# Kernel optimization log

Measured on AMD Instinct MI355X. Metric: run time of the kernel, lower is better.

The kernel has to match this reference:

```python
import jax, jax.numpy as jnp
import numpy as np

D_MODEL = 2048
H = 8
DK = D_MODEL // H          # 256
EXPAND = 2
D_INNER = EXPAND * D_MODEL  # 4096
D_STATE = 16
D_CONV = 4
DT_RANK = D_MODEL // 16     # 128
B_SZ = 8
L = 1024


def setup_inputs() -> dict:
    key = jax.random.key(0)
    ks = jax.random.split(key, 20)
    s = 0.02
    inp = {
        "imageFeature": jax.random.normal(ks[0], (B_SZ, L, D_MODEL), jnp.float32),
        "kf": jax.random.normal(ks[1], (B_SZ, L, D_MODEL), jnp.float32),
        # MHA params (4 linears with bias)
        "Wq": jax.random.normal(ks[2], (D_MODEL, D_MODEL), jnp.float32) * s,
        "bq": jnp.zeros((D_MODEL,), jnp.float32),
        "Wk": jax.random.normal(ks[3], (D_MODEL, D_MODEL), jnp.float32) * s,
        "bk": jnp.zeros((D_MODEL,), jnp.float32),
        "Wv": jax.random.normal(ks[4], (D_MODEL, D_MODEL), jnp.float32) * s,
        "bv": jnp.zeros((D_MODEL,), jnp.float32),
        "Wo": jax.random.normal(ks[5], (D_MODEL, D_MODEL), jnp.float32) * s,
        "bo": jnp.zeros((D_MODEL,), jnp.float32),
        # Mamba params
        "W_in": jax.random.normal(ks[6], (D_MODEL, 2 * D_INNER), jnp.float32) * s,
        "conv_w": jax.random.normal(ks[7], (D_INNER, D_CONV), jnp.float32) * s,
        "conv_b": jnp.zeros((D_INNER,), jnp.float32),
        "W_extra": jax.random.normal(ks[8], (D_MODEL, D_INNER), jnp.float32) * s,
        "W_xproj": jax.random.normal(ks[9], (D_INNER, DT_RANK + 2 * D_STATE), jnp.float32) * s,
        "W_dt": jax.random.normal(ks[10], (DT_RANK, D_INNER), jnp.float32) * s,
        "b_dt": jnp.full((D_INNER,), -4.6, jnp.float32),  # softplus(-4.6) ~ 0.01 init dt
        "A_log": jnp.log(jnp.broadcast_to(jnp.arange(1, D_STATE + 1, dtype=jnp.float32), (D_INNER, D_STATE))),
        "D_skip": jnp.ones((D_INNER,), jnp.float32),
        "W_out": jax.random.normal(ks[11], (D_INNER, D_MODEL), jnp.float32) * s,
    }
    return inp


def _mha(x, Wq, bq, Wk, bk, Wv, bv, Wo, bo):
    B, T, _ = x.shape
    q = (x @ Wq + bq).reshape(B, T, H, DK)
    k = (x @ Wk + bk).reshape(B, T, H, DK)
    v = (x @ Wv + bv).reshape(B, T, H, DK)
    scores = jnp.einsum("bqhd,bkhd->bhqk", q, k) / jnp.sqrt(jnp.float32(DK))
    attn = jax.nn.softmax(scores, axis=-1)
    out = jnp.einsum("bhqk,bkhd->bqhd", attn, v).reshape(B, T, D_MODEL)
    return out @ Wo + bo


def _mamba_cross(x_in, kf, W_in, conv_w, conv_b, W_extra, W_xproj, W_dt, b_dt, A_log, D_skip, W_out):
    B, T, _ = x_in.shape
    xz = x_in @ W_in                       # (B,T,2*D_INNER)
    x, z = jnp.split(xz, 2, axis=-1)
    # causal depthwise conv1d (kernel D_CONV)
    x_pad = jnp.pad(x, ((0, 0), (D_CONV - 1, 0), (0, 0)))
    x_conv = sum(conv_w[:, k] * x_pad[:, k:k + T, :] for k in range(D_CONV)) + conv_b
    x = jax.nn.silu(x_conv)               # (B,T,D_INNER)
    # dt/B/C conditioned on extra_emb (cross path)
    e = kf @ W_extra                       # (B,T,D_INNER)
    dbc = e @ W_xproj                      # (B,T,DT_RANK+2*D_STATE)
    dt = jax.nn.softplus(dbc[..., :DT_RANK] @ W_dt + b_dt)        # (B,T,D_INNER)
    Bt = dbc[..., DT_RANK:DT_RANK + D_STATE]                      # (B,T,N)
    Ct = dbc[..., DT_RANK + D_STATE:]                             # (B,T,N)
    A = -jnp.exp(A_log)                    # (D_INNER, D_STATE)

    def step(h, inputs):
        x_t, dt_t, B_t, C_t = inputs       # (B,D),(B,D),(B,N),(B,N)
        dA = jnp.exp(dt_t[..., None] * A)              # (B,D,N)
        h = dA * h + dt_t[..., None] * B_t[:, None, :] * x_t[..., None]
        y_t = jnp.einsum("bdn,bn->bd", h, C_t)
        return h, y_t

    h0 = jnp.zeros((B, D_INNER, D_STATE), x.dtype)
    xs = (x.transpose(1, 0, 2), dt.transpose(1, 0, 2),
          Bt.transpose(1, 0, 2), Ct.transpose(1, 0, 2))
    _, ys = jax.lax.scan(step, h0, xs)     # ys: (T,B,D_INNER)
    y = ys.transpose(1, 0, 2) + D_skip * x
    y = y * jax.nn.silu(z)
    return y @ W_out


def reference(imageFeature, kf, Wq, bq, Wk, bk, Wv, bv, Wo, bo,
              W_in, conv_w, conv_b, W_extra, W_xproj, W_dt, b_dt,
              A_log, D_skip, W_out):
    att_feats = _mha(imageFeature, Wq, bq, Wk, bk, Wv, bv, Wo, bo)
    src = _mamba_cross(imageFeature, kf, W_in, conv_w, conv_b, W_extra,
                       W_xproj, W_dt, b_dt, A_log, D_skip, W_out)
    return jnp.stack([att_feats, src])     # (2,B,T,D_MODEL)
```

## Files before the change

### kernel.cpp

```cpp
#include <hip/hip_runtime.h>
#include <math.h>

#define NH 8
#define DKH 256
#define SEQ 1024
#define BSZ 8
#define DMODEL 2048
#define DINNER 4096
#define DSTATE 16
#define DTRANK 128

#define MiB 1048576ULL

#define O_XZ    (0*MiB)
#define O_IMGH  (256*MiB)
#define O_IMGL  (288*MiB)
#define O_WINTH (320*MiB)
#define O_WINTL (352*MiB)
#define O_WCOMB (384*MiB)
#define O_DBC   (384*MiB + 1310720ULL)
#define O_DT    (256*MiB)
#define O_YH    (256*MiB)
#define O_YL    (320*MiB)
#define O_WOUTH (0*MiB)
#define O_WOUTL (16*MiB)
#define A_IMGH  (0*MiB)
#define A_IMGL  (32*MiB)
#define A_WQH   (64*MiB)
#define A_WQL   (72*MiB)
#define A_WKH   (80*MiB)
#define A_WKL   (88*MiB)
#define A_WVH   (96*MiB)
#define A_WVL   (104*MiB)
#define A_WOH   (112*MiB)
#define A_WOL   (120*MiB)
#define A_QH    (128*MiB)
#define A_QL    (160*MiB)
#define A_KH    (192*MiB)
#define A_KL    (224*MiB)
#define A_VTH   (256*MiB)
#define A_VTL   (288*MiB)
#define A_S     (320*MiB)
#define A_ATTH  (0*MiB)
#define A_ATTL  (32*MiB)

#define FLAG_BIAS 1
#define FLAG_SOFTPLUS 2
#define FLAG_KT 4
#define FLAG_BF16 8

typedef __attribute__((ext_vector_type(8))) short bf16x8;
typedef __attribute__((ext_vector_type(4))) float f32x4;
typedef const void __attribute__((address_space(1))) gv_t;
typedef void __attribute__((address_space(3))) lv_t;

__device__ __forceinline__ unsigned short f2bf(float x) {
    unsigned u = __float_as_uint(x);
    unsigned r = u + 0x7FFFu + ((u >> 16) & 1u);
    return (unsigned short)(r >> 16);
}
__device__ __forceinline__ float bf2f(unsigned short h) {
    return __uint_as_float((unsigned)h << 16);
}

__device__ __forceinline__ float fsilu(float x) {
    return x * __builtin_amdgcn_rcpf(1.f + __expf(-x));
}

template<int CTRL>
__device__ __forceinline__ float dppadd(float x) {
    return x + __int_as_float(__builtin_amdgcn_mov_dpp(
        __float_as_int(x), CTRL, 0xf, 0xf, true));
}

__global__ __launch_bounds__(256) void cvt_hilo(
    const float* __restrict__ in, unsigned short* __restrict__ hi,
    unsigned short* __restrict__ lo, int n4)
{
    int i = blockIdx.x * 256 + threadIdx.x;
    if (i >= n4) return;
    float4 x = ((const float4*)in)[i];
    ushort4 h, l;
    h.x = f2bf(x.x); l.x = f2bf(x.x - bf2f(h.x));
    h.y = f2bf(x.y); l.y = f2bf(x.y - bf2f(h.y));
    h.z = f2bf(x.z); l.z = f2bf(x.z - bf2f(h.z));
    h.w = f2bf(x.w); l.w = f2bf(x.w - bf2f(h.w));
    ((ushort4*)hi)[i] = h;
    ((ushort4*)lo)[i] = l;
}

__global__ __launch_bounds__(256) void tcvt(
    const float* __restrict__ W, unsigned short* __restrict__ Thi,
    unsigned short* __restrict__ Tlo, int K, int N)
{
    __shared__ float t[32][33];
    int tx = threadIdx.x & 31, ty = threadIdx.x >> 5;
    int k0 = blockIdx.y * 32, n0 = blockIdx.x * 32;
    #pragma unroll
    for (int i = 0; i < 32; i += 8)
        t[ty + i][tx] = W[(size_t)(k0 + ty + i) * N + n0 + tx];
    __syncthreads();
    #pragma unroll
    for (int i = 0; i < 32; i += 8) {
        float v = t[tx][ty + i];
        size_t o = (size_t)(n0 + ty + i) * K + k0 + tx;
        unsigned short h = f2bf(v);
        Thi[o] = h;
        Tlo[o] = f2bf(v - bf2f(h));
    }
}

__global__ __launch_bounds__(256) void ycvt(
    const float* __restrict__ xz, unsigned short* __restrict__ hi,
    unsigned short* __restrict__ lo)
{
    int i = blockIdx.x * 256 + threadIdx.x;
    int r = i >> 10, c4 = (i & 1023) << 2;
    float4 x = *(const float4*)&xz[(size_t)r * 8192 + c4];
    ushort4 h, l;
    h.x = f2bf(x.x); l.x = f2bf(x.x - bf2f(h.x));
    h.y = f2bf(x.y); l.y = f2bf(x.y - bf2f(h.y));
    h.z = f2bf(x.z); l.z = f2bf(x.z - bf2f(h.z));
    h.w = f2bf(x.w); l.w = f2bf(x.w - bf2f(h.w));
    size_t o = ((size_t)r * 4096 + c4) >> 2;
    ((ushort4*)hi)[o] = h;
    ((ushort4*)lo)[o] = l;
}

__device__ __forceinline__ void gload16(const unsigned short* g, unsigned short* l) {
    __builtin_amdgcn_global_load_lds((gv_t*)g, (lv_t*)l, 16, 0, 0);
}

__global__ __launch_bounds__(256) void gemm_mfma3(
    const unsigned short* __restrict__ Ahi, const unsigned short* __restrict__ Alo,
    const unsigned short* __restrict__ Bhi, const unsigned short* __restrict__ Blo,
    const float* __restrict__ bias, float* __restrict__ C,
    unsigned short* __restrict__ Chi, unsigned short* __restrict__ Clo,
    int M, int N, int K, int flags)
{
    __shared__ unsigned short sAh[128*32], sAl[128*32], sBh[128*32], sBl[128*32];
    int tid = threadIdx.x;
    int lane = tid & 63, wv = tid >> 6;
    int wm = wv >> 1, wn = wv & 1;
    int bm = blockIdx.y * 128, bn = blockIdx.x * 128;

    int rbase = wv * 32;
    int srow = lane >> 2;
    int scol = (lane & 3) * 8;
    const size_t aoff0 = (size_t)(bm + rbase + srow) * K + scol;
    const size_t aoff1 = aoff0 + (size_t)16 * K;
    const size_t boff0 = (size_t)(bn + rbase + srow) * K + scol;
    const size_t boff1 = boff0 + (size_t)16 * K;
    unsigned short* lA0 = &sAh[rbase * 32];
    unsigned short* lA1 = &sAh[(rbase + 16) * 32];
    unsigned short* lAl0 = &sAl[rbase * 32];
    unsigned short* lAl1 = &sAl[(rbase + 16) * 32];
    unsigned short* lB0 = &sBh[rbase * 32];
    unsigned short* lB1 = &sBh[(rbase + 16) * 32];
    unsigned short* lBl0 = &sBl[rbase * 32];
    unsigned short* lBl1 = &sBl[(rbase + 16) * 32];

    f32x4 acc[4][4];
    #pragma unroll
    for (int i = 0; i < 4; i++)
        #pragma unroll
        for (int j = 0; j < 4; j++)
            acc[i][j] = (f32x4){0.f, 0.f, 0.f, 0.f};

    int fr = lane & 15, q8 = (lane >> 4) * 8;

    for (int k0 = 0; k0 < K; k0 += 32) {
        gload16(Ahi + aoff0 + k0, lA0);
        gload16(Ahi + aoff1 + k0, lA1);
        gload16(Alo + aoff0 + k0, lAl0);
        gload16(Alo + aoff1 + k0, lAl1);
        gload16(Bhi + boff0 + k0, lB0);
        gload16(Bhi + boff1 + k0, lB1);
        gload16(Blo + boff0 + k0, lBl0);
        gload16(Blo + boff1 + k0, lBl1);
        __syncthreads();

        bf16x8 ah[4], al[4], bh[4], bl[4];
        #pragma unroll
        for (int t = 0; t < 4; t++) {
            ah[t] = *(const bf16x8*)&sAh[(wm * 64 + t * 16 + fr) * 32 + q8];
            al[t] = *(const bf16x8*)&sAl[(wm * 64 + t * 16 + fr) * 32 + q8];
            bh[t] = *(const bf16x8*)&sBh[(wn * 64 + t * 16 + fr) * 32 + q8];
            bl[t] = *(const bf16x8*)&sBl[(wn * 64 + t * 16 + fr) * 32 + q8];
        }
        #pragma unroll
        for (int i = 0; i < 4; i++)
            #pragma unroll
            for (int j = 0; j < 4; j++) {
                acc[i][j] = __builtin_amdgcn_mfma_f32_16x16x32_bf16(ah[i], bh[j], acc[i][j], 0, 0, 0);
                acc[i][j] = __builtin_amdgcn_mfma_f32_16x16x32_bf16(al[i], bh[j], acc[i][j], 0, 0, 0);
                acc[i][j] = __builtin_amdgcn_mfma_f32_16x16x32_bf16(ah[i], bl[j], acc[i][j], 0, 0, 0);
            }
        __syncthreads();
    }

    int q4 = (lane >> 4) * 4, c16 = lane & 15;
    #pragma unroll
    for (int i = 0; i < 4; i++)
        #pragma unroll
        for (int j = 0; j < 4; j++) {
            f32x4 v = acc[i][j];
            int col = bn + wn * 64 + j * 16 + c16;
            float bv = (flags & FLAG_BIAS) ? bias[col] : 0.f;
            #pragma unroll
            for (int r = 0; r < 4; r++) {
                int row = bm + wm * 64 + i * 16 + q4 + r;
                float val = v[r] + bv;
                if (flags & FLAG_BF16) {
                    size_t o;
                    if (flags & FLAG_KT) {
                        int bi = row >> 10, jj = row & 1023;
                        int hd = col >> 8, dk2 = col & 255;
                        o = ((size_t)((bi * NH + hd) * DKH + dk2)) * SEQ + jj;
                    } else {
                        o = (size_t)row * N + col;
                    }
                    unsigned short hv = f2bf(val);
                    Chi[o] = hv;
                    Clo[o] = f2bf(val - bf2f(hv));
                } else if (flags & FLAG_KT) {
                    int bi = row >> 10, jj = row & 1023;
                    int hd = col >> 8, dk2 = col & 255;
                    C[((size_t)((bi * NH + hd) * DKH + dk2)) * SEQ + jj] = val;
                } else {
                    C[(size_t)row * N + col] = val;
                }
            }
        }
}

__global__ __launch_bounds__(256) void gemm_att3(
    const unsigned short* __restrict__ Ahi, const unsigned short* __restrict__ Alo,
    const unsigned short* __restrict__ Bhi, const unsigned short* __restrict__ Blo,
    float* __restrict__ Cf, unsigned short* __restrict__ Ohi, unsigned short* __restrict__ Olo,
    int K, int lda, int ldb, int chunk_base, int mode)
{
    __shared__ unsigned short sAh[128*32], sAl[128*32], sBh[128*32], sBl[128*32];
    int tid = threadIdx.x;
    int lane = tid & 63, wv = tid >> 6;
    int wm = wv >> 1, wn = wv & 1;
    int bm = blockIdx.y * 128, bn = blockIdx.x * 128;
    int z = blockIdx.z;
    int g = chunk_base + z;

    size_t abase, bbase;
    if (mode == 0) {
        abase = (size_t)(g >> 3) * (1024 * 2048) + (size_t)(g & 7) * 256;
        bbase = abase;
    } else {
        abase = (size_t)z * (1024 * 2048);
        bbase = (size_t)g * (256 * 1024);
    }

    int rbase = wv * 32;
    int srow = lane >> 2;
    int scol = (lane & 3) * 8;
    const size_t aoff0 = abase + (size_t)(bm + rbase + srow) * lda + scol;
    const size_t aoff1 = aoff0 + (size_t)16 * lda;
    const size_t boff0 = bbase + (size_t)(bn + rbase + srow) * ldb + scol;
    const size_t boff1 = boff0 + (size_t)16 * ldb;
    unsigned short* lA0 = &sAh[rbase * 32];
    unsigned short* lA1 = &sAh[(rbase + 16) * 32];
    unsigned short* lAl0 = &sAl[rbase * 32];
    unsigned short* lAl1 = &sAl[(rbase + 16) * 32];
    unsigned short* lB0 = &sBh[rbase * 32];
    unsigned short* lB1 = &sBh[(rbase + 16) * 32];
    unsigned short* lBl0 = &sBl[rbase * 32];
    unsigned short* lBl1 = &sBl[(rbase + 16) * 32];

    f32x4 acc[4][4];
    #pragma unroll
    for (int i = 0; i < 4; i++)
        #pragma unroll
        for (int j = 0; j < 4; j++)
            acc[i][j] = (f32x4){0.f, 0.f, 0.f, 0.f};

    int fr = lane & 15, q8 = (lane >> 4) * 8;

    for (int k0 = 0; k0 < K; k0 += 32) {
        gload16(Ahi + aoff0 + k0, lA0);
        gload16(Ahi + aoff1 + k0, lA1);
        gload16(Alo + aoff0 + k0, lAl0);
        gload16(Alo + aoff1 + k0, lAl1);
        gload16(Bhi + boff0 + k0, lB0);
        gload16(Bhi + boff1 + k0, lB1);
        gload16(Blo + boff0 + k0, lBl0);
        gload16(Blo + boff1 + k0, lBl1);
        __syncthreads();

        bf16x8 ah[4], al[4], bh[4], bl[4];
        #pragma unroll
        for (int t = 0; t < 4; t++) {
            ah[t] = *(const bf16x8*)&sAh[(wm * 64 + t * 16 + fr) * 32 + q8];
            al[t] = *(const bf16x8*)&sAl[(wm * 64 + t * 16 + fr) * 32 + q8];
            bh[t] = *(const bf16x8*)&sBh[(wn * 64 + t * 16 + fr) * 32 + q8];
            bl[t] = *(const bf16x8*)&sBl[(wn * 64 + t * 16 + fr) * 32 + q8];
        }
        #pragma unroll
        for (int i = 0; i < 4; i++)
            #pragma unroll
            for (int j = 0; j < 4; j++) {
                acc[i][j] = __builtin_amdgcn_mfma_f32_16x16x32_bf16(ah[i], bh[j], acc[i][j], 0, 0, 0);
                acc[i][j] = __builtin_amdgcn_mfma_f32_16x16x32_bf16(al[i], bh[j], acc[i][j], 0, 0, 0);
                acc[i][j] = __builtin_amdgcn_mfma_f32_16x16x32_bf16(ah[i], bl[j], acc[i][j], 0, 0, 0);
            }
        __syncthreads();
    }

    int q4 = (lane >> 4) * 4, c16 = lane & 15;
    #pragma unroll
    for (int i = 0; i < 4; i++)
        #pragma unroll
        for (int j = 0; j < 4; j++) {
            f32x4 v = acc[i][j];
            int col = bn + wn * 64 + j * 16 + c16;
            #pragma unroll
            for (int r = 0; r < 4; r++) {
                int row = bm + wm * 64 + i * 16 + q4 + r;
                float val = v[r];
                if (mode == 0) {
                    Cf[(size_t)z * (1024 * 1024) + (size_t)row * 1024 + col] = val * 0.0625f;
                } else {
                    size_t o = ((size_t)((g >> 3) * 1024 + row)) * 2048 + (size_t)(g & 7) * 256 + col;
                    unsigned short hv = f2bf(val);
                    Ohi[o] = hv;
                    Olo[o] = f2bf(val - bf2f(hv));
                }
            }
        }
}

__global__ __launch_bounds__(256) void softmax_rows(float* __restrict__ S)
{
    int lane = threadIdx.x & 63, wid = threadIdx.x >> 6;
    size_t row = (size_t)blockIdx.x * 4 + wid;
    float* rp = S + row * 1024;

    float4 x[4];
    float m = -1e30f;
    #pragma unroll
    for (int w = 0; w < 4; w++) {
        x[w] = *(const float4*)&rp[w * 256 + lane * 4];
        m = fmaxf(m, fmaxf(fmaxf(x[w].x, x[w].y), fmaxf(x[w].z, x[w].w)));
    }
    #pragma unroll
    for (int off = 1; off < 64; off <<= 1) m = fmaxf(m, __shfl_xor(m, off));

    float s = 0.f;
    #pragma unroll
    for (int w = 0; w < 4; w++) {
        x[w].x = __expf(x[w].x - m);
        x[w].y = __expf(x[w].y - m);
        x[w].z = __expf(x[w].z - m);
        x[w].w = __expf(x[w].w - m);
        s += x[w].x + x[w].y + x[w].z + x[w].w;
    }
    #pragma unroll
    for (int off = 1; off < 64; off <<= 1) s += __shfl_xor(s, off);
    float inv = 1.f / s;

    unsigned short* hp = (unsigned short*)rp;
    unsigned short* lp = hp + 1024;
    #pragma unroll
    for (int w = 0; w < 4; w++) {
        float a0 = x[w].x * inv, a1 = x[w].y * inv;
        float a2 = x[w].z * inv, a3 = x[w].w * inv;
        ushort4 h, l;
        h.x = f2bf(a0); l.x = f2bf(a0 - bf2f(h.x));
        h.y = f2bf(a1); l.y = f2bf(a1 - bf2f(h.y));
        h.z = f2bf(a2); l.z = f2bf(a2 - bf2f(h.z));
        h.w = f2bf(a3); l.w = f2bf(a3 - bf2f(h.w));
        int c = w * 256 + lane * 4;
        *(ushort4*)&hp[c] = h;
        *(ushort4*)&lp[c] = l;
    }
}

#define BM 64
#define BN 64
#define BK 16
__global__ __launch_bounds__(256) void gemm_f32(
    const float* __restrict__ A, const float* __restrict__ B,
    const float* __restrict__ bias, float* __restrict__ C,
    int M, int N, int K, int lda, int ldb, int ldc, int flags)
{
    __shared__ float As[BK][BM + 4];
    __shared__ float Bs[BK][BN + 4];
    int tid = threadIdx.x;
    int tm = tid >> 4, tn = tid & 15;
    int bm = blockIdx.y * BM, bn = blockIdx.x * BN;
    float acc[4][4] = {};

    for (int k0 = 0; k0 < K; k0 += BK) {
        #pragma unroll
        for (int i = 0; i < 4; i++) {
            int idx = tid + i * 256;
            int r = idx >> 4, c = idx & 15;
            int gr = bm + r, gc = k0 + c;
            float v = 0.f;
            if (gr < M && gc < K) v = A[(size_t)gr * lda + gc];
            As[c][r] = v;
        }
        #pragma unroll
        for (int i = 0; i < 4; i++) {
            int idx = tid + i * 256;
            int r = idx >> 6, c = idx & 63;
            int gr = k0 + r, gc = bn + c;
            float v = 0.f;
            if (gr < K && gc < N) v = B[(size_t)gr * ldb + gc];
            Bs[r][c] = v;
        }
        __syncthreads();
        #pragma unroll
        for (int kk = 0; kk < BK; kk++) {
            float4 a4 = *(const float4*)&As[kk][tm * 4];
            float4 b4 = *(const float4*)&Bs[kk][tn * 4];
            float av[4] = {a4.x, a4.y, a4.z, a4.w};
            float bv[4] = {b4.x, b4.y, b4.z, b4.w};
            #pragma unroll
            for (int i = 0; i < 4; i++)
                #pragma unroll
                for (int j = 0; j < 4; j++)
                    acc[i][j] += av[i] * bv[j];
        }
        __syncthreads();
    }

    #pragma unroll
    for (int i = 0; i < 4; i++) {
        int row = bm + tm * 4 + i;
        if (row >= M) continue;
        #pragma unroll
        for (int j = 0; j < 4; j++) {
            int col = bn + tn * 4 + j;
            if (col >= N) continue;
            float val = acc[i][j];
            if (flags & FLAG_BIAS) val += bias[col];
            if (flags & FLAG_SOFTPLUS) val = (val > 20.f) ? val : log1pf(__expf(val));
            C[(size_t)row * ldc + col] = val;
        }
    }
}

__global__ __launch_bounds__(256) void repack_bc(float* __restrict__ dbc)
{
    int i = blockIdx.x * 256 + threadIdx.x;
    int n = i & 15;
    int row = i >> 4;
    float B = dbc[(size_t)row * 160 + DTRANK + n];
    float C = dbc[(size_t)row * 160 + DTRANK + DSTATE + n];
    float2 p; p.x = B; p.y = C;
    ((float2*)&dbc[(size_t)row * 160])[n] = p;
}

__global__ __launch_bounds__(256) void scan_prep(
    const float* __restrict__ xz_r, float* __restrict__ xz_w,
    const float* __restrict__ conv_w, const float* __restrict__ conv_b,
    float* __restrict__ xs_out)
{
    int d = blockIdx.x * 256 + threadIdx.x;
    int t0 = blockIdx.y * 128;
    int b = blockIdx.z;
    float cw0 = conv_w[d * 4 + 0], cw1 = conv_w[d * 4 + 1];
    float cw2 = conv_w[d * 4 + 2], cw3 = conv_w[d * 4 + 3];
    float cb = conv_b[d];
    size_t base = (size_t)b * SEQ * 8192 + d;

    float w0 = 0.f, w1 = 0.f, w2 = 0.f;
    if (t0 > 0) {
        w0 = xz_r[base + (size_t)(t0 - 3) * 8192];
        w1 = xz_r[base + (size_t)(t0 - 2) * 8192];
        w2 = xz_r[base + (size_t)(t0 - 1) * 8192];
    }
    for (int t = t0; t < t0 + 128; t++) {
        float xr = xz_r[base + (size_t)t * 8192];
        float xc = cw0 * w0 + cw1 * w1 + cw2 * w2 + cw3 * xr + cb;
        w0 = w1; w1 = w2; w2 = xr;
        xs_out[((size_t)b * SEQ + t) * 4096 + d] = fsilu(xc);
        float zv = xz_r[base + (size_t)t * 8192 + DINNER];
        xz_w[base + (size_t)t * 8192 + DINNER] = fsilu(zv);
    }
}

__global__ __launch_bounds__(256) void mamba_scan(
    float* __restrict__ xz, const float* __restrict__ dt,
    const float* __restrict__ bc, const float* __restrict__ A_log,
    const float* __restrict__ D_skip, const float* __restrict__ xs)
{
    int tid = threadIdx.x;
    int n = tid & 15;
    int dd = tid >> 4;
    int gb = blockIdx.x;
    int b = gb >> 8;
    int d = ((gb & 255) << 4) + dd;

    float A_n = -__expf(A_log[d * DSTATE + n]);
    float dsk = D_skip[d];

    float h = 0.f;
    size_t rowx = (size_t)b * SEQ * 8192 + d;
    size_t rowd = (size_t)b * SEQ * 4096 + d;
    size_t rowbc = (size_t)b * SEQ * 160;

    #pragma unroll 2
    for (int t = 0; t < SEQ; t++) {
        float xv  = xs[rowd + (size_t)t * 4096];
        float dtv = dt[rowd + (size_t)t * 4096];
        float2 bcv = *(const float2*)&bc[rowbc + (size_t)t * 160 + 2 * n];
        float g   = xz[rowx + (size_t)t * 8192 + DINNER];

        float dA = __expf(dtv * A_n);
        h = dA * h + (dtv * xv) * bcv.x;
        float p = h * bcv.y;
        p = dppadd<0xB1>(p);
        p = dppadd<0x4E>(p);
        p = dppadd<0x141>(p);
        p = dppadd<0x140>(p);
        if (n == 0) {
            float y = (p + dsk * xv) * g;
            xz[rowx + (size_t)t * 8192] = y;
        }
    }
}

extern "C" void kernel_launch(void* const* d_in, const int* in_sizes, int n_in,
                              void* d_out, int out_size, void* d_ws, size_t ws_size,
                              hipStream_t stream) {
    const float* imgF   = (const float*)d_in[0];
    const float* kf     = (const float*)d_in[1];
    const float* Wq     = (const float*)d_in[2];
    const float* bq     = (const float*)d_in[3];
    const float* Wk     = (const float*)d_in[4];
    const float* bk     = (const float*)d_in[5];
    const float* Wv     = (const float*)d_in[6];
    const float* bv     = (const float*)d_in[7];
    const float* Wo     = (const float*)d_in[8];
    const float* bo     = (const float*)d_in[9];
    const float* W_in   = (const float*)d_in[10];
    const float* conv_w = (const float*)d_in[11];
    const float* conv_b = (const float*)d_in[12];
    const float* W_extra= (const float*)d_in[13];
    const float* W_xproj= (const float*)d_in[14];
    const float* W_dt   = (const float*)d_in[15];
    const float* b_dt   = (const float*)d_in[16];
    const float* A_log  = (const float*)d_in[17];
    const float* D_skip = (const float*)d_in[18];
    const float* W_out  = (const float*)d_in[19];
    float* out = (float*)d_out;
    char* W = (char*)d_ws;

    #define WS_F(off) ((float*)(W + (off)))
    #define WS_U(off) ((unsigned short*)(W + (off)))

    dim3 blk(256);
    auto gg = [](int M, int N) { return dim3((N + BN - 1) / BN, (M + BM - 1) / BM); };

    cvt_hilo<<<dim3(16384), blk, 0, stream>>>(imgF, WS_U(O_IMGH), WS_U(O_IMGL), 4194304);
    tcvt<<<dim3(8192/32, 2048/32), blk, 0, stream>>>(W_in, WS_U(O_WINTH), WS_U(O_WINTL), 2048, 8192);
    gemm_mfma3<<<dim3(64, 64), blk, 0, stream>>>(WS_U(O_IMGH), WS_U(O_IMGL),
        WS_U(O_WINTH), WS_U(O_WINTL), nullptr, WS_F(O_XZ), nullptr, nullptr,
        8192, 8192, 2048, 0);
    gemm_f32<<<gg(2048, 160), blk, 0, stream>>>(W_extra, W_xproj, nullptr, WS_F(O_WCOMB),
        2048, 160, 4096, 4096, 160, 160, 0);
    gemm_f32<<<gg(8192, 160), blk, 0, stream>>>(kf, WS_F(O_WCOMB), nullptr, WS_F(O_DBC),
        8192, 160, 2048, 2048, 160, 160, 0);
    gemm_f32<<<gg(8192, 4096), blk, 0, stream>>>(WS_F(O_DBC), W_dt, b_dt, WS_F(O_DT),
        8192, 4096, 128, 160, 4096, 4096, FLAG_BIAS | FLAG_SOFTPLUS);
    repack_bc<<<dim3(512), blk, 0, stream>>>(WS_F(O_DBC));
    scan_prep<<<dim3(16, 8, 8), blk, 0, stream>>>(WS_F(O_XZ), WS_F(O_XZ),
        conv_w, conv_b, out);
    mamba_scan<<<dim3(2048), blk, 0, stream>>>(WS_F(O_XZ), WS_F(O_DT), WS_F(O_DBC),
        A_log, D_skip, out);
    ycvt<<<dim3(32768), blk, 0, stream>>>(WS_F(O_XZ), WS_U(O_YH), WS_U(O_YL));
    tcvt<<<dim3(2048/32, 4096/32), blk, 0, stream>>>(W_out, WS_U(O_WOUTH), WS_U(O_WOUTL), 4096, 2048);
    gemm_mfma3<<<dim3(16, 64), blk, 0, stream>>>(WS_U(O_YH), WS_U(O_YL),
        WS_U(O_WOUTH), WS_U(O_WOUTL), nullptr, out + 16777216, nullptr, nullptr,
        8192, 2048, 4096, 0);

    cvt_hilo<<<dim3(16384), blk, 0, stream>>>(imgF, WS_U(A_IMGH), WS_U(A_IMGL), 4194304);
    tcvt<<<dim3(64, 64), blk, 0, stream>>>(Wq, WS_U(A_WQH), WS_U(A_WQL), 2048, 2048);
    tcvt<<<dim3(64, 64), blk, 0, stream>>>(Wk, WS_U(A_WKH), WS_U(A_WKL), 2048, 2048);
    tcvt<<<dim3(64, 64), blk, 0, stream>>>(Wv, WS_U(A_WVH), WS_U(A_WVL), 2048, 2048);
    tcvt<<<dim3(64, 64), blk, 0, stream>>>(Wo, WS_U(A_WOH), WS_U(A_WOL), 2048, 2048);
    gemm_mfma3<<<dim3(16, 64), blk, 0, stream>>>(WS_U(A_IMGH), WS_U(A_IMGL),
        WS_U(A_WQH), WS_U(A_WQL), bq, nullptr, WS_U(A_QH), WS_U(A_QL),
        8192, 2048, 2048, FLAG_BIAS | FLAG_BF16);
    gemm_mfma3<<<dim3(16, 64), blk, 0, stream>>>(WS_U(A_IMGH), WS_U(A_IMGL),
        WS_U(A_WKH), WS_U(A_WKL), bk, nullptr, WS_U(A_KH), WS_U(A_KL),
        8192, 2048, 2048, FLAG_BIAS | FLAG_BF16);
    gemm_mfma3<<<dim3(16, 64), blk, 0, stream>>>(WS_U(A_IMGH), WS_U(A_IMGL),
        WS_U(A_WVH), WS_U(A_WVL), bv, nullptr, WS_U(A_VTH), WS_U(A_VTL),
        8192, 2048, 2048, FLAG_BIAS | FLAG_BF16 | FLAG_KT);
    for (int c = 0; c < 4; c++) {
        gemm_att3<<<dim3(8, 8, 16), blk, 0, stream>>>(WS_U(A_QH), WS_U(A_QL),
            WS_U(A_KH), WS_U(A_KL), WS_F(A_S), nullptr, nullptr,
            256, 2048, 2048, c * 16, 0);
        softmax_rows<<<dim3(4096), blk, 0, stream>>>(WS_F(A_S));
        gemm_att3<<<dim3(2, 8, 16), blk, 0, stream>>>(
            (unsigned short*)WS_F(A_S), (unsigned short*)WS_F(A_S) + 1024,
            WS_U(A_VTH), WS_U(A_VTL), nullptr, WS_U(A_ATTH), WS_U(A_ATTL),
            1024, 2048, 1024, c * 16, 1);
    }
    gemm_mfma3<<<dim3(16, 64), blk, 0, stream>>>(WS_U(A_ATTH), WS_U(A_ATTL),
        WS_U(A_WOH), WS_U(A_WOL), bo, out, nullptr, nullptr,
        8192, 2048, 2048, FLAG_BIAS);
}
```

Measured before the change: 5.367 ms.

## Transpose dt and conv output for scan, move dt projection to MFMA

The dt projection moves from the fp32 GEMM to the split-bf16 MFMA GEMM, whose epilogue applies softplus and writes dt in a time-contiguous (b,d,t) layout. The conv+SiLU step becomes a tiled shared-memory kernel that also writes a transposed x layout. The scan stages 64-step chunks of x, dt and B/C through LDS with coalesced vector loads instead of strided per-step global loads. The silu(z) gating moves into the y conversion kernel. The goal is to cut strided memory traffic in the latency-bound scan and the slow fp32 GEMM, at the cost of more workspace buffers and an extra pack kernel.

```diff
diff --git a/kernel.cpp b/kernel.cpp
--- a/kernel.cpp
+++ b/kernel.cpp
@@ -19,7 +19,11 @@
 #define O_WINTL (352*MiB)
 #define O_WCOMB (384*MiB)
 #define O_DBC   (384*MiB + 1310720ULL)
-#define O_DT    (256*MiB)
+#define O_DBCH  (256*MiB)
+#define O_DBCL  (259*MiB)
+#define O_WDTH  (262*MiB)
+#define O_WDTL  (264*MiB)
+#define O_XST   (256*MiB)
 #define O_YH    (256*MiB)
 #define O_YL    (320*MiB)
 #define O_WOUTH (0*MiB)
@@ -48,6 +52,7 @@
 #define FLAG_SOFTPLUS 2
 #define FLAG_KT 4
 #define FLAG_BF16 8
+#define FLAG_DTT 16
 
 typedef __attribute__((ext_vector_type(8))) short bf16x8;
 typedef __attribute__((ext_vector_type(4))) float f32x4;
@@ -110,6 +115,23 @@
     }
 }
 
+__global__ __launch_bounds__(256) void pack_dbc128(
+    const float* __restrict__ dbc, unsigned short* __restrict__ hi,
+    unsigned short* __restrict__ lo)
+{
+    int i = blockIdx.x * 256 + threadIdx.x;
+    int r = i >> 5, c4 = (i & 31) << 2;
+    float4 x = *(const float4*)&dbc[(size_t)r * 160 + c4];
+    ushort4 h, l;
+    h.x = f2bf(x.x); l.x = f2bf(x.x - bf2f(h.x));
+    h.y = f2bf(x.y); l.y = f2bf(x.y - bf2f(h.y));
+    h.z = f2bf(x.z); l.z = f2bf(x.z - bf2f(h.z));
+    h.w = f2bf(x.w); l.w = f2bf(x.w - bf2f(h.w));
+    size_t o = ((size_t)r * 128 + c4) >> 2;
+    ((ushort4*)hi)[o] = h;
+    ((ushort4*)lo)[o] = l;
+}
+
 __global__ __launch_bounds__(256) void ycvt(
     const float* __restrict__ xz, unsigned short* __restrict__ hi,
     unsigned short* __restrict__ lo)
@@ -117,6 +139,9 @@
     int i = blockIdx.x * 256 + threadIdx.x;
     int r = i >> 10, c4 = (i & 1023) << 2;
     float4 x = *(const float4*)&xz[(size_t)r * 8192 + c4];
+    float4 z = *(const float4*)&xz[(size_t)r * 8192 + DINNER + c4];
+    x.x *= fsilu(z.x); x.y *= fsilu(z.y);
+    x.z *= fsilu(z.z); x.w *= fsilu(z.w);
     ushort4 h, l;
     h.x = f2bf(x.x); l.x = f2bf(x.x - bf2f(h.x));
     h.y = f2bf(x.y); l.y = f2bf(x.y - bf2f(h.y));
@@ -211,7 +236,10 @@
             for (int r = 0; r < 4; r++) {
                 int row = bm + wm * 64 + i * 16 + q4 + r;
                 float val = v[r] + bv;
-                if (flags & FLAG_BF16) {
+                if (flags & FLAG_DTT) {
+                    float sp = (val > 20.f) ? val : log1pf(__expf(val));
+                    C[((size_t)(row >> 10) * 4096 + col) * 1024 + (row & 1023)] = sp;
+                } else if (flags & FLAG_BF16) {
                     size_t o;
                     if (flags & FLAG_KT) {
                         int bi = row >> 10, jj = row & 1023;
@@ -458,72 +486,108 @@
     ((float2*)&dbc[(size_t)row * 160])[n] = p;
 }
 
-__global__ __launch_bounds__(256) void scan_prep(
-    const float* __restrict__ xz_r, float* __restrict__ xz_w,
-    const float* __restrict__ conv_w, const float* __restrict__ conv_b,
-    float* __restrict__ xs_out)
-{
-    int d = blockIdx.x * 256 + threadIdx.x;
-    int t0 = blockIdx.y * 128;
-    int b = blockIdx.z;
+__global__ __launch_bounds__(256) void conv_prep(
+    const float* __restrict__ xz, float* __restrict__ xsT,
+    const float* __restrict__ conv_w, const float* __restrict__ conv_b)
+{
+    __shared__ float sx[67][68];
+    int tid = threadIdx.x;
+    int d0 = blockIdx.x * 64;
+    int t0 = blockIdx.y * 64;
+    int tloc0 = t0 & 1023;
+
+    int lr = tid >> 2;
+    int lc = (tid & 3) * 16;
+    for (int rr = lr; rr < 67; rr += 64) {
+        int tg = t0 - 3 + rr;
+        bool ok = (tloc0 != 0) || (rr >= 3);
+        #pragma unroll
+        for (int c = 0; c < 16; c += 4) {
+            float4 v = ok ? *(const float4*)&xz[(size_t)tg * 8192 + d0 + lc + c]
+                          : (float4){0.f, 0.f, 0.f, 0.f};
+            *(float4*)&sx[rr][lc + c] = v;
+        }
+    }
+    __syncthreads();
+
+    int dr = tid >> 2;
+    int tq = (tid & 3) * 16;
+    int d = d0 + dr;
     float cw0 = conv_w[d * 4 + 0], cw1 = conv_w[d * 4 + 1];
     float cw2 = conv_w[d * 4 + 2], cw3 = conv_w[d * 4 + 3];
     float cb = conv_b[d];
-    size_t base = (size_t)b * SEQ * 8192 + d;
-
-    float w0 = 0.f, w1 = 0.f, w2 = 0.f;
-    if (t0 > 0) {
-        w0 = xz_r[base + (size_t)(t0 - 3) * 8192];
-        w1 = xz_r[base + (size_t)(t0 - 2) * 8192];
-        w2 = xz_r[base + (size_t)(t0 - 1) * 8192];
-    }
-    for (int t = t0; t < t0 + 128; t++) {
-        float xr = xz_r[base + (size_t)t * 8192];
-        float xc = cw0 * w0 + cw1 * w1 + cw2 * w2 + cw3 * xr + cb;
-        w0 = w1; w1 = w2; w2 = xr;
-        xs_out[((size_t)b * SEQ + t) * 4096 + d] = fsilu(xc);
-        float zv = xz_r[base + (size_t)t * 8192 + DINNER];
-        xz_w[base + (size_t)t * 8192 + DINNER] = fsilu(zv);
-    }
+
+    float x0 = sx[tq + 0][dr], x1 = sx[tq + 1][dr], x2 = sx[tq + 2][dr];
+    float o[16];
+    #pragma unroll
+    for (int tt = 0; tt < 16; tt++) {
+        float x3 = sx[tq + tt + 3][dr];
+        float xc = cw0 * x0 + cw1 * x1 + cw2 * x2 + cw3 * x3 + cb;
+        o[tt] = fsilu(xc);
+        x0 = x1; x1 = x2; x2 = x3;
+    }
+    size_t ob = ((size_t)(t0 >> 10) * 4096 + d) * 1024 + tloc0 + tq;
+    #pragma unroll
+    for (int c = 0; c < 16; c += 4)
+        *(float4*)&xsT[ob + c] = (float4){o[c], o[c+1], o[c+2], o[c+3]};
 }
 
 __global__ __launch_bounds__(256) void mamba_scan(
-    float* __restrict__ xz, const float* __restrict__ dt,
+    float* __restrict__ xz, const float* __restrict__ dtT,
     const float* __restrict__ bc, const float* __restrict__ A_log,
-    const float* __restrict__ D_skip, const float* __restrict__ xs)
-{
+    const float* __restrict__ D_skip, const float* __restrict__ xsT)
+{
+    __shared__ float sxs[16 * 68];
+    __shared__ float sdt[16 * 68];
+    __shared__ float sbc[64 * 32];
+
     int tid = threadIdx.x;
     int n = tid & 15;
     int dd = tid >> 4;
     int gb = blockIdx.x;
     int b = gb >> 8;
-    int d = ((gb & 255) << 4) + dd;
+    int d0 = (gb & 255) << 4;
+    int d = d0 + dd;
 
     float A_n = -__expf(A_log[d * DSTATE + n]);
     float dsk = D_skip[d];
-
     float h = 0.f;
-    size_t rowx = (size_t)b * SEQ * 8192 + d;
-    size_t rowd = (size_t)b * SEQ * 4096 + d;
+
+    size_t baseT = ((size_t)b * 4096 + d0) * 1024;
     size_t rowbc = (size_t)b * SEQ * 160;
-
-    #pragma unroll 2
-    for (int t = 0; t < SEQ; t++) {
-        float xv  = xs[rowd + (size_t)t * 4096];
-        float dtv = dt[rowd + (size_t)t * 4096];
-        float2 bcv = *(const float2*)&bc[rowbc + (size_t)t * 160 + 2 * n];
-        float g   = xz[rowx + (size_t)t * 8192 + DINNER];
-
-        float dA = __expf(dtv * A_n);
-        h = dA * h + (dtv * xv) * bcv.x;
-        float p = h * bcv.y;
-        p = dppadd<0xB1>(p);
-        p = dppadd<0x4E>(p);
-        p = dppadd<0x141>(p);
-        p = dppadd<0x140>(p);
-        if (n == 0) {
-            float y = (p + dsk * xv) * g;
-            xz[rowx + (size_t)t * 8192] = y;
+    size_t rowx  = (size_t)b * SEQ * 8192 + d;
+
+    int sr = tid >> 4;
+    int sc = (tid & 15) * 4;
+    int br = tid >> 2;
+    int bq = (tid & 3) * 8;
+
+    for (int t0 = 0; t0 < SEQ; t0 += 64) {
+        float4 vx = *(const float4*)&xsT[baseT + (size_t)sr * 1024 + t0 + sc];
+        float4 vd = *(const float4*)&dtT[baseT + (size_t)sr * 1024 + t0 + sc];
+        float4 v0 = *(const float4*)&bc[rowbc + (size_t)(t0 + br) * 160 + bq];
+        float4 v1 = *(const float4*)&bc[rowbc + (size_t)(t0 + br) * 160 + bq + 4];
+        __syncthreads();
+        *(float4*)&sxs[sr * 68 + sc] = vx;
+        *(float4*)&sdt[sr * 68 + sc] = vd;
+        *(float4*)&sbc[br * 32 + bq] = v0;
+        *(float4*)&sbc[br * 32 + bq + 4] = v1;
+        __syncthreads();
+
+        #pragma unroll 4
+        for (int tl = 0; tl < 64; tl++) {
+            float xv  = sxs[dd * 68 + tl];
+            float dtv = sdt[dd * 68 + tl];
+            float2 bcv = *(const float2*)&sbc[tl * 32 + 2 * n];
+            float dA = __expf(dtv * A_n);
+            h = dA * h + (dtv * xv) * bcv.x;
+            float p = h * bcv.y;
+            p = dppadd<0xB1>(p);
+            p = dppadd<0x4E>(p);
+            p = dppadd<0x141>(p);
+            p = dppadd<0x140>(p);
+            if (n == 0)
+                xz[rowx + (size_t)(t0 + tl) * 8192] = p + dsk * xv;
         }
     }
 }
@@ -569,13 +633,15 @@
         2048, 160, 4096, 4096, 160, 160, 0);
     gemm_f32<<<gg(8192, 160), blk, 0, stream>>>(kf, WS_F(O_WCOMB), nullptr, WS_F(O_DBC),
         8192, 160, 2048, 2048, 160, 160, 0);
-    gemm_f32<<<gg(8192, 4096), blk, 0, stream>>>(WS_F(O_DBC), W_dt, b_dt, WS_F(O_DT),
-        8192, 4096, 128, 160, 4096, 4096, FLAG_BIAS | FLAG_SOFTPLUS);
+    pack_dbc128<<<dim3(1024), blk, 0, stream>>>(WS_F(O_DBC), WS_U(O_DBCH), WS_U(O_DBCL));
     repack_bc<<<dim3(512), blk, 0, stream>>>(WS_F(O_DBC));
-    scan_prep<<<dim3(16, 8, 8), blk, 0, stream>>>(WS_F(O_XZ), WS_F(O_XZ),
-        conv_w, conv_b, out);
-    mamba_scan<<<dim3(2048), blk, 0, stream>>>(WS_F(O_XZ), WS_F(O_DT), WS_F(O_DBC),
-        A_log, D_skip, out);
+    tcvt<<<dim3(4096/32, 128/32), blk, 0, stream>>>(W_dt, WS_U(O_WDTH), WS_U(O_WDTL), 128, 4096);
+    gemm_mfma3<<<dim3(32, 64), blk, 0, stream>>>(WS_U(O_DBCH), WS_U(O_DBCL),
+        WS_U(O_WDTH), WS_U(O_WDTL), b_dt, out, nullptr, nullptr,
+        8192, 4096, 128, FLAG_BIAS | FLAG_DTT);
+    conv_prep<<<dim3(64, 128), blk, 0, stream>>>(WS_F(O_XZ), WS_F(O_XST), conv_w, conv_b);
+    mamba_scan<<<dim3(2048), blk, 0, stream>>>(WS_F(O_XZ), out, WS_F(O_DBC),
+        A_log, D_skip, WS_F(O_XST));
     ycvt<<<dim3(32768), blk, 0, stream>>>(WS_F(O_XZ), WS_U(O_YH), WS_U(O_YL));
     tcvt<<<dim3(2048/32, 4096/32), blk, 0, stream>>>(W_out, WS_U(O_WOUTH), WS_U(O_WOUTL), 4096, 2048);
     gemm_mfma3<<<dim3(16, 64), blk, 0, stream>>>(WS_U(O_YH), WS_U(O_YL),
```

New measurement: 4.701 ms. 12.4% less time.
